# Performance work log

Hardware: AMD Instinct MI355X
Metric: run time of the kernel (lower is better)

Reference implementation:

```python
import jax, jax.numpy as jnp
import numpy as np

N = 50000   # nodes
E = 800000  # edges
D = 128     # input_dim
H = 128     # hidden_dim
C = 40      # output_dim (classes)


def setup_inputs() -> dict:
    key = jax.random.key(0)
    ks = jax.random.split(key, 8)
    x = jax.random.normal(ks[0], (N, D), dtype=jnp.float32)
    edge_index = jax.random.randint(ks[1], (2, E), 0, N, dtype=jnp.int32)
    sD = 1.0 / np.sqrt(D)
    sH = 1.0 / np.sqrt(H)
    W1 = jax.random.uniform(ks[2], (D, H), jnp.float32, -sD, sD)
    b1 = jnp.zeros((H,), jnp.float32)
    W2 = jax.random.uniform(ks[3], (H, H), jnp.float32, -sH, sH)
    b2 = jnp.zeros((H,), jnp.float32)
    W3 = jax.random.uniform(ks[4], (H, C), jnp.float32, -sH, sH)
    b3 = jnp.zeros((C,), jnp.float32)
    return {"x": x, "edge_index": edge_index,
            "W1": W1, "b1": b1, "W2": W2, "b2": b2, "W3": W3, "b3": b3}


def reference(x, edge_index, W1, b1, W2, b2, W3, b3):
    # GCNConv: out = D^{-1/2} (A + I) D^{-1/2} (x @ W) + b
    src = edge_index[0]
    dst = edge_index[1]
    loop = jnp.arange(N, dtype=src.dtype)
    src_f = jnp.concatenate([src, loop])  # [E+N] with self-loops
    dst_f = jnp.concatenate([dst, loop])
    deg = jax.ops.segment_sum(jnp.ones(E + N, x.dtype), dst_f, num_segments=N)
    dinv = jax.lax.rsqrt(jnp.maximum(deg, 1.0))  # deg >= 1 due to self-loops
    norm = dinv[src_f] * dinv[dst_f]  # [E+N]

    def conv(h, W, b):
        h = h @ W                       # [N, F_out]
        msg = h[src_f] * norm[:, None]  # [E+N, F_out] gathered messages
        return jax.ops.segment_sum(msg, dst_f, num_segments=N) + b

    h = jax.nn.relu(conv(x, W1, b1))
    h = jax.nn.relu(conv(h, W2, b2))  # dropout is identity in eval mode
    return conv(h, W3, b3)
```

## Files before the change

kernel.cpp:

```cpp
#include <hip/hip_runtime.h>

typedef unsigned short ushort_t;
typedef unsigned int uint_t;


__global__ void k_deg_count(const int* __restrict__ ei, int* __restrict__ deg, int E) {
    int e = blockIdx.x * blockDim.x + threadIdx.x;
    if (e < E) atomicAdd(&deg[ei[E + e]], 1);
}

__global__ void k_bsum(const int* __restrict__ deg, int* __restrict__ bsum, int n) {
    __shared__ int s[256];
    int t = threadIdx.x;
    int i = blockIdx.x * 256 + t;
    s[t] = (i < n) ? deg[i] : 0;
    __syncthreads();
    for (int off = 128; off > 0; off >>= 1) {
        if (t < off) s[t] += s[t + off];
        __syncthreads();
    }
    if (t == 0) bsum[blockIdx.x] = s[0];
}

__global__ void k_bscan(int* __restrict__ bsum, int* __restrict__ tot, int nb) {
    __shared__ int s[1024];
    int t = threadIdx.x;
    int v = (t < nb) ? bsum[t] : 0;
    s[t] = v;
    __syncthreads();
    for (int off = 1; off < 1024; off <<= 1) {
        int u = (t >= off) ? s[t - off] : 0;
        __syncthreads();
        s[t] += u;
        __syncthreads();
    }
    if (t < nb) bsum[t] = s[t] - v;
    if (t == nb - 1) tot[0] = s[t];
}

__global__ void k_rowptr(const int* __restrict__ deg, const int* __restrict__ bsum,
                         int* __restrict__ rowptr, int* __restrict__ cursor,
                         float* __restrict__ dinv, int n) {
    __shared__ int s[256];
    int t = threadIdx.x;
    int i = blockIdx.x * 256 + t;
    int v = (i < n) ? deg[i] : 0;
    s[t] = v;
    __syncthreads();
    for (int off = 1; off < 256; off <<= 1) {
        int u = (t >= off) ? s[t - off] : 0;
        __syncthreads();
        s[t] += u;
        __syncthreads();
    }
    if (i < n) {
        int ex = bsum[blockIdx.x] + s[t] - v;
        rowptr[i] = ex;
        cursor[i] = ex;
        dinv[i] = rsqrtf((float)(v + 1));
    }
}

__global__ __launch_bounds__(256) void k_fill(const int* __restrict__ ei,
                                              int* __restrict__ cursor,
                                              const float* __restrict__ dinv,
                                              int2* __restrict__ csr, int E, int n) {
    const int xcd = blockIdx.x & 7;
    const int e = (blockIdx.x >> 3) * 256 + threadIdx.x;
    if (e >= E) return;
    int d = ei[E + e];
    const int lo = (int)(((long long)xcd * n) >> 3);
    const int hi = (int)(((long long)(xcd + 1) * n) >> 3);
    if (d < lo || d >= hi) return;
    int s = ei[e];
    int pos = atomicAdd(&cursor[d], 1);
    int2 p;
    p.x = s;
    p.y = __float_as_int(dinv[s] * dinv[d]);
    csr[pos] = p;
}

__device__ __forceinline__ ushort_t f2bf_rne(float f) {
    uint_t u = __float_as_uint(f);
    u += 0x7fffu + ((u >> 16) & 1u);
    return (ushort_t)(u >> 16);
}
__device__ __forceinline__ float bflo(uint_t u) {
    return __uint_as_float(u << 16);
}
__device__ __forceinline__ float bfhi(uint_t u) {
    return __uint_as_float(u & 0xffff0000u);
}

__global__ __launch_bounds__(256) void k_gemm128(const float* __restrict__ X,
                                                 const float* __restrict__ W,
                                                 ushort_t* __restrict__ Y, int N) {
    __shared__ float sX[32][132];
    __shared__ float sW[32][128];
    const int tid = threadIdx.x;
    const int bm = blockIdx.x * 128;
    const int m0 = (tid >> 4) * 8;
    const int c4 = (tid & 15) * 4;
    const int xf = tid & 7;
    float acc[8][8] = {};
    for (int k0 = 0; k0 < 128; k0 += 32) {
        #pragma unroll
        for (int it = 0; it < 4; ++it) {
            int i = tid + it * 256;
            int row = bm + (i >> 3);
            int rc = min(row, N - 1);
            float4 v = *(const float4*)(X + (size_t)rc * 128 + k0 + xf * 4);
            int m = i >> 3;
            sX[xf * 4 + 0][m] = v.x;
            sX[xf * 4 + 1][m] = v.y;
            sX[xf * 4 + 2][m] = v.z;
            sX[xf * 4 + 3][m] = v.w;
        }
        #pragma unroll
        for (int it = 0; it < 4; ++it) {
            int i = tid + it * 256;
            int wr = i >> 5;
            int wf = i & 31;
            *(float4*)(&sW[wr][wf * 4]) =
                *(const float4*)(W + (size_t)(k0 + wr) * 128 + wf * 4);
        }
        __syncthreads();
        #pragma unroll
        for (int kk = 0; kk < 32; ++kk) {
            float4 a0 = *(const float4*)(&sX[kk][m0]);
            float4 a1 = *(const float4*)(&sX[kk][m0 + 4]);
            float4 b0 = *(const float4*)(&sW[kk][c4]);
            float4 b1 = *(const float4*)(&sW[kk][64 + c4]);
            float av[8] = {a0.x, a0.y, a0.z, a0.w, a1.x, a1.y, a1.z, a1.w};
            float bv[8] = {b0.x, b0.y, b0.z, b0.w, b1.x, b1.y, b1.z, b1.w};
            #pragma unroll
            for (int r = 0; r < 8; ++r)
                #pragma unroll
                for (int c = 0; c < 8; ++c)
                    acc[r][c] = fmaf(av[r], bv[c], acc[r][c]);
        }
        __syncthreads();
    }
    #pragma unroll
    for (int r = 0; r < 8; ++r) {
        int row = bm + m0 + r;
        if (row < N) {
            ushort4 o0 = {f2bf_rne(acc[r][0]), f2bf_rne(acc[r][1]),
                          f2bf_rne(acc[r][2]), f2bf_rne(acc[r][3])};
            ushort4 o1 = {f2bf_rne(acc[r][4]), f2bf_rne(acc[r][5]),
                          f2bf_rne(acc[r][6]), f2bf_rne(acc[r][7])};
            *(ushort4*)(Y + (size_t)row * 128 + c4)      = o0;
            *(ushort4*)(Y + (size_t)row * 128 + 64 + c4) = o1;
        }
    }
}

__global__ __launch_bounds__(256) void k_gemm40(const float* __restrict__ X,
                                                const float* __restrict__ W,
                                                ushort_t* __restrict__ Y, int N) {
    __shared__ float sX[32][132];
    __shared__ float sW[32][40];
    const int tid = threadIdx.x;
    const int bm = blockIdx.x * 128;
    const int m0 = (tid >> 3) * 4;
    const int n0 = (tid & 7) * 5;
    const int xf = tid & 7;
    float acc[4][5] = {};
    for (int k0 = 0; k0 < 128; k0 += 32) {
        #pragma unroll
        for (int it = 0; it < 4; ++it) {
            int i = tid + it * 256;
            int row = bm + (i >> 3);
            int rc = min(row, N - 1);
            float4 v = *(const float4*)(X + (size_t)rc * 128 + k0 + xf * 4);
            int m = i >> 3;
            sX[xf * 4 + 0][m] = v.x;
            sX[xf * 4 + 1][m] = v.y;
            sX[xf * 4 + 2][m] = v.z;
            sX[xf * 4 + 3][m] = v.w;
        }
        for (int i = tid; i < 320; i += 256) {
            int wr = i / 10;
            int wf = i - wr * 10;
            *(float4*)(&sW[wr][wf * 4]) =
                *(const float4*)(W + (size_t)(k0 + wr) * 40 + wf * 4);
        }
        __syncthreads();
        #pragma unroll
        for (int kk = 0; kk < 32; ++kk) {
            float4 a = *(const float4*)(&sX[kk][m0]);
            float av[4] = {a.x, a.y, a.z, a.w};
            #pragma unroll
            for (int c = 0; c < 5; ++c) {
                float b = sW[kk][n0 + c];
                #pragma unroll
                for (int r = 0; r < 4; ++r)
                    acc[r][c] = fmaf(av[r], b, acc[r][c]);
            }
        }
        __syncthreads();
    }
    #pragma unroll
    for (int r = 0; r < 4; ++r) {
        int row = bm + m0 + r;
        if (row < N) {
            #pragma unroll
            for (int c = 0; c < 5; ++c)
                Y[(size_t)row * 64 + n0 + c] = f2bf_rne(acc[r][c]);
        }
    }
}

template <bool RELU>
__global__ __launch_bounds__(256) void k_agg128(
        const ushort_t* __restrict__ XW, const int* __restrict__ rowptr,
        const int2* __restrict__ csr, const float* __restrict__ dinv,
        const float* __restrict__ bias, float* __restrict__ out, int n) {
    const int lane = threadIdx.x & 63;
    const int wv = __builtin_amdgcn_readfirstlane(threadIdx.x >> 6);
    const int d = blockIdx.x * 4 + wv;
    if (d >= n) return;
    const uint_t* xw = (const uint_t*)XW;
    float dv = dinv[d];
    float w0 = dv * dv;
    uint_t sq = xw[(size_t)d * 64 + lane];
    float2 a;
    a.x = w0 * bflo(sq);
    a.y = w0 * bfhi(sq);
    int j = rowptr[d], end = rowptr[d + 1];
    for (; j + 8 <= end; j += 8) {
        int2 p0 = csr[j + 0], p1 = csr[j + 1], p2 = csr[j + 2], p3 = csr[j + 3];
        int2 p4 = csr[j + 4], p5 = csr[j + 5], p6 = csr[j + 6], p7 = csr[j + 7];
        uint_t u0 = xw[(size_t)p0.x * 64 + lane];
        uint_t u1 = xw[(size_t)p1.x * 64 + lane];
        uint_t u2 = xw[(size_t)p2.x * 64 + lane];
        uint_t u3 = xw[(size_t)p3.x * 64 + lane];
        uint_t u4 = xw[(size_t)p4.x * 64 + lane];
        uint_t u5 = xw[(size_t)p5.x * 64 + lane];
        uint_t u6 = xw[(size_t)p6.x * 64 + lane];
        uint_t u7 = xw[(size_t)p7.x * 64 + lane];
        float w0e = __int_as_float(p0.y), w1e = __int_as_float(p1.y);
        float w2e = __int_as_float(p2.y), w3e = __int_as_float(p3.y);
        float w4e = __int_as_float(p4.y), w5e = __int_as_float(p5.y);
        float w6e = __int_as_float(p6.y), w7e = __int_as_float(p7.y);
        a.x = fmaf(w0e, bflo(u0), a.x); a.y = fmaf(w0e, bfhi(u0), a.y);
        a.x = fmaf(w1e, bflo(u1), a.x); a.y = fmaf(w1e, bfhi(u1), a.y);
        a.x = fmaf(w2e, bflo(u2), a.x); a.y = fmaf(w2e, bfhi(u2), a.y);
        a.x = fmaf(w3e, bflo(u3), a.x); a.y = fmaf(w3e, bfhi(u3), a.y);
        a.x = fmaf(w4e, bflo(u4), a.x); a.y = fmaf(w4e, bfhi(u4), a.y);
        a.x = fmaf(w5e, bflo(u5), a.x); a.y = fmaf(w5e, bfhi(u5), a.y);
        a.x = fmaf(w6e, bflo(u6), a.x); a.y = fmaf(w6e, bfhi(u6), a.y);
        a.x = fmaf(w7e, bflo(u7), a.x); a.y = fmaf(w7e, bfhi(u7), a.y);
    }
    for (; j < end; ++j) {
        int2 p = csr[j];
        float we = __int_as_float(p.y);
        uint_t u = xw[(size_t)p.x * 64 + lane];
        a.x = fmaf(we, bflo(u), a.x);
        a.y = fmaf(we, bfhi(u), a.y);
    }
    float2 b = ((const float2*)bias)[lane];
    a.x += b.x; a.y += b.y;
    if (RELU) {
        a.x = fmaxf(a.x, 0.f);
        a.y = fmaxf(a.y, 0.f);
    }
    ((float2*)out)[(size_t)d * 64 + lane] = a;
}

__global__ __launch_bounds__(256) void k_agg40(
        const ushort_t* __restrict__ XW, const int* __restrict__ rowptr,
        const int2* __restrict__ csr, const float* __restrict__ dinv,
        const float* __restrict__ bias, float* __restrict__ out, int n) {
    const int lane = threadIdx.x & 31;
    const int sub  = threadIdx.x >> 5;
    const int d = blockIdx.x * 8 + sub;
    if (d >= n || lane >= 20) return;
    const uint_t* xw = (const uint_t*)XW;
    float dv = dinv[d];
    float w0 = dv * dv;
    uint_t sq = xw[(size_t)d * 32 + lane];
    float2 a;
    a.x = w0 * bflo(sq);
    a.y = w0 * bfhi(sq);
    int j = rowptr[d], end = rowptr[d + 1];
    for (; j + 4 <= end; j += 4) {
        int2 p0 = csr[j + 0], p1 = csr[j + 1], p2 = csr[j + 2], p3 = csr[j + 3];
        uint_t u0 = xw[(size_t)p0.x * 32 + lane];
        uint_t u1 = xw[(size_t)p1.x * 32 + lane];
        uint_t u2 = xw[(size_t)p2.x * 32 + lane];
        uint_t u3 = xw[(size_t)p3.x * 32 + lane];
        float w0e = __int_as_float(p0.y), w1e = __int_as_float(p1.y);
        float w2e = __int_as_float(p2.y), w3e = __int_as_float(p3.y);
        a.x = fmaf(w0e, bflo(u0), a.x); a.y = fmaf(w0e, bfhi(u0), a.y);
        a.x = fmaf(w1e, bflo(u1), a.x); a.y = fmaf(w1e, bfhi(u1), a.y);
        a.x = fmaf(w2e, bflo(u2), a.x); a.y = fmaf(w2e, bfhi(u2), a.y);
        a.x = fmaf(w3e, bflo(u3), a.x); a.y = fmaf(w3e, bfhi(u3), a.y);
    }
    for (; j < end; ++j) {
        int2 p = csr[j];
        float we = __int_as_float(p.y);
        uint_t u = xw[(size_t)p.x * 32 + lane];
        a.x = fmaf(we, bflo(u), a.x);
        a.y = fmaf(we, bfhi(u), a.y);
    }
    float2 b = ((const float2*)bias)[lane];
    a.x += b.x; a.y += b.y;
    ((float2*)out)[(size_t)d * 20 + lane] = a;
}

static inline int cdiv(long long a, int b) { return (int)((a + b - 1) / b); }

extern "C" void kernel_launch(void* const* d_in, const int* in_sizes, int n_in,
                              void* d_out, int out_size, void* d_ws, size_t ws_size,
                              hipStream_t stream) {
    const float* x  = (const float*)d_in[0];
    const int*   ei = (const int*)d_in[1];
    const float* W1 = (const float*)d_in[2];
    const float* b1 = (const float*)d_in[3];
    const float* W2 = (const float*)d_in[4];
    const float* b2 = (const float*)d_in[5];
    const float* W3 = (const float*)d_in[6];
    const float* b3 = (const float*)d_in[7];
    float* out = (float*)d_out;

    const int N = in_sizes[0] / 128;
    const int E = in_sizes[1] / 2;

    char* ws = (char*)d_ws;
    int*   deg    = (int*)ws;                 ws += (size_t)N * 4;
    int*   rowptr = (int*)ws;                 ws += (size_t)(N + 1) * 4;
    int*   cursor = (int*)ws;                 ws += (size_t)N * 4;
    float* dinv   = (float*)ws;               ws += (size_t)N * 4;
    int*   bsum   = (int*)ws;                 ws += (size_t)1024 * 4;
    ws = (char*)(((uintptr_t)ws + 127) & ~(uintptr_t)127);
    int2*  csr    = (int2*)ws;                ws += (size_t)E * 8;
    char*  bufA   = ws;                       ws += (size_t)N * 128 * 4;
    float* bufB   = (float*)ws;

    const int BT = 256;
    const int nb = cdiv(N, 256);

    hipMemsetAsync(deg, 0, (size_t)N * 4, stream);
    k_deg_count<<<cdiv(E, BT), BT, 0, stream>>>(ei, deg, E);
    k_bsum<<<nb, 256, 0, stream>>>(deg, bsum, N);
    k_bscan<<<1, 1024, 0, stream>>>(bsum, rowptr + N, nb);
    k_rowptr<<<nb, 256, 0, stream>>>(deg, bsum, rowptr, cursor, dinv, N);
    k_fill<<<cdiv(E, BT) * 8, 256, 0, stream>>>(ei, cursor, dinv, csr, E, N);

    k_gemm128<<<cdiv(N, 128), 256, 0, stream>>>(x, W1, (ushort_t*)bufA, N);
    k_agg128<true><<<cdiv(N, 4), 256, 0, stream>>>((const ushort_t*)bufA, rowptr, csr, dinv, b1, bufB, N);
    k_gemm128<<<cdiv(N, 128), 256, 0, stream>>>(bufB, W2, (ushort_t*)bufA, N);
    k_agg128<true><<<cdiv(N, 4), 256, 0, stream>>>((const ushort_t*)bufA, rowptr, csr, dinv, b2, bufB, N);
    k_gemm40<<<cdiv(N, 128), 256, 0, stream>>>(bufB, W3, (ushort_t*)bufA, N);
    k_agg40<<<cdiv(N, 8), 256, 0, stream>>>((const ushort_t*)bufA, rowptr, csr, dinv, b3, out, N);
}
```

Baseline: 321.8 us.

## Merge three-pass scan into single-pass decoupled lookback; deepen aggregation unroll

```diff
diff --git a/kernel.cpp b/kernel.cpp
--- a/kernel.cpp
+++ b/kernel.cpp
@@ -9,41 +9,14 @@
     if (e < E) atomicAdd(&deg[ei[E + e]], 1);
 }
 
-__global__ void k_bsum(const int* __restrict__ deg, int* __restrict__ bsum, int n) {
+__global__ __launch_bounds__(256) void k_scan(
+        const int* __restrict__ deg, unsigned long long* __restrict__ partials,
+        int* __restrict__ rowptr, int* __restrict__ cursor,
+        float* __restrict__ dinv, int n) {
     __shared__ int s[256];
-    int t = threadIdx.x;
-    int i = blockIdx.x * 256 + t;
-    s[t] = (i < n) ? deg[i] : 0;
-    __syncthreads();
-    for (int off = 128; off > 0; off >>= 1) {
-        if (t < off) s[t] += s[t + off];
-        __syncthreads();
-    }
-    if (t == 0) bsum[blockIdx.x] = s[0];
-}
-
-__global__ void k_bscan(int* __restrict__ bsum, int* __restrict__ tot, int nb) {
-    __shared__ int s[1024];
-    int t = threadIdx.x;
-    int v = (t < nb) ? bsum[t] : 0;
-    s[t] = v;
-    __syncthreads();
-    for (int off = 1; off < 1024; off <<= 1) {
-        int u = (t >= off) ? s[t - off] : 0;
-        __syncthreads();
-        s[t] += u;
-        __syncthreads();
-    }
-    if (t < nb) bsum[t] = s[t] - v;
-    if (t == nb - 1) tot[0] = s[t];
-}
-
-__global__ void k_rowptr(const int* __restrict__ deg, const int* __restrict__ bsum,
-                         int* __restrict__ rowptr, int* __restrict__ cursor,
-                         float* __restrict__ dinv, int n) {
-    __shared__ int s[256];
-    int t = threadIdx.x;
-    int i = blockIdx.x * 256 + t;
+    __shared__ int sprefix;
+    const int b = blockIdx.x, t = threadIdx.x;
+    const int i = b * 256 + t;
     int v = (i < n) ? deg[i] : 0;
     s[t] = v;
     __syncthreads();
@@ -53,11 +26,32 @@
         s[t] += u;
         __syncthreads();
     }
+    if (t == 0) {
+        unsigned long long bs = (unsigned long long)s[255];
+        __hip_atomic_store(&partials[b], (bs << 2) | 1ull,
+                           __ATOMIC_RELEASE, __HIP_MEMORY_SCOPE_AGENT);
+        long long acc = 0;
+        for (int k = b - 1; k >= 0; ) {
+            unsigned long long p = __hip_atomic_load(&partials[k],
+                    __ATOMIC_ACQUIRE, __HIP_MEMORY_SCOPE_AGENT);
+            unsigned st = (unsigned)(p & 3ull);
+            if (st == 0) continue;
+            acc += (long long)(p >> 2);
+            if (st == 2) break;
+            --k;
+        }
+        __hip_atomic_store(&partials[b],
+                (((unsigned long long)(acc + (long long)bs)) << 2) | 2ull,
+                __ATOMIC_RELEASE, __HIP_MEMORY_SCOPE_AGENT);
+        sprefix = (int)acc;
+    }
+    __syncthreads();
     if (i < n) {
-        int ex = bsum[blockIdx.x] + s[t] - v;
+        int ex = sprefix + s[t] - v;
         rowptr[i] = ex;
         cursor[i] = ex;
         dinv[i] = rsqrtf((float)(v + 1));
+        if (i == n - 1) rowptr[n] = ex + v;
     }
 }
 
@@ -228,29 +222,33 @@
     a.x = w0 * bflo(sq);
     a.y = w0 * bfhi(sq);
     int j = rowptr[d], end = rowptr[d + 1];
+    for (; j + 16 <= end; j += 16) {
+        int2 p[16];
+        #pragma unroll
+        for (int q = 0; q < 16; ++q) p[q] = csr[j + q];
+        uint_t u[16];
+        #pragma unroll
+        for (int q = 0; q < 16; ++q) u[q] = xw[(size_t)p[q].x * 64 + lane];
+        #pragma unroll
+        for (int q = 0; q < 16; ++q) {
+            float we = __int_as_float(p[q].y);
+            a.x = fmaf(we, bflo(u[q]), a.x);
+            a.y = fmaf(we, bfhi(u[q]), a.y);
+        }
+    }
     for (; j + 8 <= end; j += 8) {
-        int2 p0 = csr[j + 0], p1 = csr[j + 1], p2 = csr[j + 2], p3 = csr[j + 3];
-        int2 p4 = csr[j + 4], p5 = csr[j + 5], p6 = csr[j + 6], p7 = csr[j + 7];
-        uint_t u0 = xw[(size_t)p0.x * 64 + lane];
-        uint_t u1 = xw[(size_t)p1.x * 64 + lane];
-        uint_t u2 = xw[(size_t)p2.x * 64 + lane];
-        uint_t u3 = xw[(size_t)p3.x * 64 + lane];
-        uint_t u4 = xw[(size_t)p4.x * 64 + lane];
-        uint_t u5 = xw[(size_t)p5.x * 64 + lane];
-        uint_t u6 = xw[(size_t)p6.x * 64 + lane];
-        uint_t u7 = xw[(size_t)p7.x * 64 + lane];
-        float w0e = __int_as_float(p0.y), w1e = __int_as_float(p1.y);
-        float w2e = __int_as_float(p2.y), w3e = __int_as_float(p3.y);
-        float w4e = __int_as_float(p4.y), w5e = __int_as_float(p5.y);
-        float w6e = __int_as_float(p6.y), w7e = __int_as_float(p7.y);
-        a.x = fmaf(w0e, bflo(u0), a.x); a.y = fmaf(w0e, bfhi(u0), a.y);
-        a.x = fmaf(w1e, bflo(u1), a.x); a.y = fmaf(w1e, bfhi(u1), a.y);
-        a.x = fmaf(w2e, bflo(u2), a.x); a.y = fmaf(w2e, bfhi(u2), a.y);
-        a.x = fmaf(w3e, bflo(u3), a.x); a.y = fmaf(w3e, bfhi(u3), a.y);
-        a.x = fmaf(w4e, bflo(u4), a.x); a.y = fmaf(w4e, bfhi(u4), a.y);
-        a.x = fmaf(w5e, bflo(u5), a.x); a.y = fmaf(w5e, bfhi(u5), a.y);
-        a.x = fmaf(w6e, bflo(u6), a.x); a.y = fmaf(w6e, bfhi(u6), a.y);
-        a.x = fmaf(w7e, bflo(u7), a.x); a.y = fmaf(w7e, bfhi(u7), a.y);
+        int2 p[8];
+        #pragma unroll
+        for (int q = 0; q < 8; ++q) p[q] = csr[j + q];
+        uint_t u[8];
+        #pragma unroll
+        for (int q = 0; q < 8; ++q) u[q] = xw[(size_t)p[q].x * 64 + lane];
+        #pragma unroll
+        for (int q = 0; q < 8; ++q) {
+            float we = __int_as_float(p[q].y);
+            a.x = fmaf(we, bflo(u[q]), a.x);
+            a.y = fmaf(we, bfhi(u[q]), a.y);
+        }
     }
     for (; j < end; ++j) {
         int2 p = csr[j];
@@ -272,9 +270,9 @@
         const ushort_t* __restrict__ XW, const int* __restrict__ rowptr,
         const int2* __restrict__ csr, const float* __restrict__ dinv,
         const float* __restrict__ bias, float* __restrict__ out, int n) {
-    const int lane = threadIdx.x & 31;
-    const int sub  = threadIdx.x >> 5;
-    const int d = blockIdx.x * 8 + sub;
+    const int lane = threadIdx.x & 63;
+    const int wv = __builtin_amdgcn_readfirstlane(threadIdx.x >> 6);
+    const int d = blockIdx.x * 4 + wv;
     if (d >= n || lane >= 20) return;
     const uint_t* xw = (const uint_t*)XW;
     float dv = dinv[d];
@@ -284,18 +282,33 @@
     a.x = w0 * bflo(sq);
     a.y = w0 * bfhi(sq);
     int j = rowptr[d], end = rowptr[d + 1];
-    for (; j + 4 <= end; j += 4) {
-        int2 p0 = csr[j + 0], p1 = csr[j + 1], p2 = csr[j + 2], p3 = csr[j + 3];
-        uint_t u0 = xw[(size_t)p0.x * 32 + lane];
-        uint_t u1 = xw[(size_t)p1.x * 32 + lane];
-        uint_t u2 = xw[(size_t)p2.x * 32 + lane];
-        uint_t u3 = xw[(size_t)p3.x * 32 + lane];
-        float w0e = __int_as_float(p0.y), w1e = __int_as_float(p1.y);
-        float w2e = __int_as_float(p2.y), w3e = __int_as_float(p3.y);
-        a.x = fmaf(w0e, bflo(u0), a.x); a.y = fmaf(w0e, bfhi(u0), a.y);
-        a.x = fmaf(w1e, bflo(u1), a.x); a.y = fmaf(w1e, bfhi(u1), a.y);
-        a.x = fmaf(w2e, bflo(u2), a.x); a.y = fmaf(w2e, bfhi(u2), a.y);
-        a.x = fmaf(w3e, bflo(u3), a.x); a.y = fmaf(w3e, bfhi(u3), a.y);
+    for (; j + 16 <= end; j += 16) {
+        int2 p[16];
+        #pragma unroll
+        for (int q = 0; q < 16; ++q) p[q] = csr[j + q];
+        uint_t u[16];
+        #pragma unroll
+        for (int q = 0; q < 16; ++q) u[q] = xw[(size_t)p[q].x * 32 + lane];
+        #pragma unroll
+        for (int q = 0; q < 16; ++q) {
+            float we = __int_as_float(p[q].y);
+            a.x = fmaf(we, bflo(u[q]), a.x);
+            a.y = fmaf(we, bfhi(u[q]), a.y);
+        }
+    }
+    for (; j + 8 <= end; j += 8) {
+        int2 p[8];
+        #pragma unroll
+        for (int q = 0; q < 8; ++q) p[q] = csr[j + q];
+        uint_t u[8];
+        #pragma unroll
+        for (int q = 0; q < 8; ++q) u[q] = xw[(size_t)p[q].x * 32 + lane];
+        #pragma unroll
+        for (int q = 0; q < 8; ++q) {
+            float we = __int_as_float(p[q].y);
+            a.x = fmaf(we, bflo(u[q]), a.x);
+            a.y = fmaf(we, bfhi(u[q]), a.y);
+        }
     }
     for (; j < end; ++j) {
         int2 p = csr[j];
@@ -326,26 +339,25 @@
 
     const int N = in_sizes[0] / 128;
     const int E = in_sizes[1] / 2;
+    const int nb = cdiv(N, 256);
 
     char* ws = (char*)d_ws;
     int*   deg    = (int*)ws;                 ws += (size_t)N * 4;
+    unsigned long long* partials = (unsigned long long*)ws;
+                                              ws += (size_t)nb * 8;
     int*   rowptr = (int*)ws;                 ws += (size_t)(N + 1) * 4;
     int*   cursor = (int*)ws;                 ws += (size_t)N * 4;
     float* dinv   = (float*)ws;               ws += (size_t)N * 4;
-    int*   bsum   = (int*)ws;                 ws += (size_t)1024 * 4;
     ws = (char*)(((uintptr_t)ws + 127) & ~(uintptr_t)127);
     int2*  csr    = (int2*)ws;                ws += (size_t)E * 8;
     char*  bufA   = ws;                       ws += (size_t)N * 128 * 4;
     float* bufB   = (float*)ws;
 
     const int BT = 256;
-    const int nb = cdiv(N, 256);
-
-    hipMemsetAsync(deg, 0, (size_t)N * 4, stream);
+
+    hipMemsetAsync(deg, 0, (size_t)N * 4 + (size_t)nb * 8, stream);
     k_deg_count<<<cdiv(E, BT), BT, 0, stream>>>(ei, deg, E);
-    k_bsum<<<nb, 256, 0, stream>>>(deg, bsum, N);
-    k_bscan<<<1, 1024, 0, stream>>>(bsum, rowptr + N, nb);
-    k_rowptr<<<nb, 256, 0, stream>>>(deg, bsum, rowptr, cursor, dinv, N);
+    k_scan<<<nb, 256, 0, stream>>>(deg, partials, rowptr, cursor, dinv, N);
     k_fill<<<cdiv(E, BT) * 8, 256, 0, stream>>>(ei, cursor, dinv, csr, E, N);
 
     k_gemm128<<<cdiv(N, 128), 256, 0, stream>>>(x, W1, (ushort_t*)bufA, N);
@@ -353,5 +365,5 @@
     k_gemm128<<<cdiv(N, 128), 256, 0, stream>>>(bufB, W2, (ushort_t*)bufA, N);
     k_agg128<true><<<cdiv(N, 4), 256, 0, stream>>>((const ushort_t*)bufA, rowptr, csr, dinv, b2, bufB, N);
     k_gemm40<<<cdiv(N, 128), 256, 0, stream>>>(bufB, W3, (ushort_t*)bufA, N);
-    k_agg40<<<cdiv(N, 8), 256, 0, stream>>>((const ushort_t*)bufA, rowptr, csr, dinv, b3, out, N);
-}
+    k_agg40<<<cdiv(N, 4), 256, 0, stream>>>((const ushort_t*)bufA, rowptr, csr, dinv, b3, out, N);
+}
```

Result: slower. 358.3 us (+11.4%).

## Replace three-kernel prefix scan with single-pass decoupled look-back scan

Applied to the files above, without the earlier changes.

```diff
diff --git a/kernel.cpp b/kernel.cpp
--- a/kernel.cpp
+++ b/kernel.cpp
@@ -9,41 +9,14 @@
     if (e < E) atomicAdd(&deg[ei[E + e]], 1);
 }
 
-__global__ void k_bsum(const int* __restrict__ deg, int* __restrict__ bsum, int n) {
+__global__ __launch_bounds__(256) void k_scan(
+        const int* __restrict__ deg, unsigned long long* __restrict__ partials,
+        int* __restrict__ rowptr, int* __restrict__ cursor,
+        float* __restrict__ dinv, int n) {
     __shared__ int s[256];
-    int t = threadIdx.x;
-    int i = blockIdx.x * 256 + t;
-    s[t] = (i < n) ? deg[i] : 0;
-    __syncthreads();
-    for (int off = 128; off > 0; off >>= 1) {
-        if (t < off) s[t] += s[t + off];
-        __syncthreads();
-    }
-    if (t == 0) bsum[blockIdx.x] = s[0];
-}
-
-__global__ void k_bscan(int* __restrict__ bsum, int* __restrict__ tot, int nb) {
-    __shared__ int s[1024];
-    int t = threadIdx.x;
-    int v = (t < nb) ? bsum[t] : 0;
-    s[t] = v;
-    __syncthreads();
-    for (int off = 1; off < 1024; off <<= 1) {
-        int u = (t >= off) ? s[t - off] : 0;
-        __syncthreads();
-        s[t] += u;
-        __syncthreads();
-    }
-    if (t < nb) bsum[t] = s[t] - v;
-    if (t == nb - 1) tot[0] = s[t];
-}
-
-__global__ void k_rowptr(const int* __restrict__ deg, const int* __restrict__ bsum,
-                         int* __restrict__ rowptr, int* __restrict__ cursor,
-                         float* __restrict__ dinv, int n) {
-    __shared__ int s[256];
-    int t = threadIdx.x;
-    int i = blockIdx.x * 256 + t;
+    __shared__ int sprefix;
+    const int b = blockIdx.x, t = threadIdx.x;
+    const int i = b * 256 + t;
     int v = (i < n) ? deg[i] : 0;
     s[t] = v;
     __syncthreads();
@@ -53,11 +26,57 @@
         s[t] += u;
         __syncthreads();
     }
+    if (t == 0) {
+        __hip_atomic_store(&partials[b],
+                ((unsigned long long)s[255] << 2) | 1ull,
+                __ATOMIC_RELEASE, __HIP_MEMORY_SCOPE_AGENT);
+        if (b == 0) {
+            __hip_atomic_store(&partials[0],
+                    ((unsigned long long)s[255] << 2) | 2ull,
+                    __ATOMIC_RELEASE, __HIP_MEMORY_SCOPE_AGENT);
+            sprefix = 0;
+        }
+    }
+    if (b > 0 && t < 64) {
+        int acc = 0;
+        int k = b - 1;
+        for (;;) {
+            int idx = k - t;
+            unsigned long long p;
+            unsigned st;
+            do {
+                if (idx >= 0) {
+                    p = __hip_atomic_load(&partials[idx],
+                            __ATOMIC_ACQUIRE, __HIP_MEMORY_SCOPE_AGENT);
+                } else {
+                    p = 2ull;
+                }
+                st = (unsigned)(p & 3ull);
+            } while (st == 0);
+            unsigned long long bal = __ballot(st == 2);
+            int L = (bal != 0) ? (__ffsll((unsigned long long)bal) - 1) : 64;
+            int val = (int)(p >> 2);
+            int contrib = (t <= L) ? val : 0;
+            #pragma unroll
+            for (int o = 32; o > 0; o >>= 1) contrib += __shfl_down(contrib, o);
+            if (t == 0) acc += contrib;
+            if (L < 64) break;
+            k -= 64;
+        }
+        if (t == 0) {
+            __hip_atomic_store(&partials[b],
+                    (((unsigned long long)(acc + s[255])) << 2) | 2ull,
+                    __ATOMIC_RELEASE, __HIP_MEMORY_SCOPE_AGENT);
+            sprefix = acc;
+        }
+    }
+    __syncthreads();
     if (i < n) {
-        int ex = bsum[blockIdx.x] + s[t] - v;
+        int ex = sprefix + s[t] - v;
         rowptr[i] = ex;
         cursor[i] = ex;
         dinv[i] = rsqrtf((float)(v + 1));
+        if (i == n - 1) rowptr[n] = ex + v;
     }
 }
 
@@ -326,26 +345,25 @@
 
     const int N = in_sizes[0] / 128;
     const int E = in_sizes[1] / 2;
+    const int nb = cdiv(N, 256);
 
     char* ws = (char*)d_ws;
     int*   deg    = (int*)ws;                 ws += (size_t)N * 4;
+    unsigned long long* partials = (unsigned long long*)ws;
+                                              ws += (size_t)nb * 8;
     int*   rowptr = (int*)ws;                 ws += (size_t)(N + 1) * 4;
     int*   cursor = (int*)ws;                 ws += (size_t)N * 4;
     float* dinv   = (float*)ws;               ws += (size_t)N * 4;
-    int*   bsum   = (int*)ws;                 ws += (size_t)1024 * 4;
     ws = (char*)(((uintptr_t)ws + 127) & ~(uintptr_t)127);
     int2*  csr    = (int2*)ws;                ws += (size_t)E * 8;
     char*  bufA   = ws;                       ws += (size_t)N * 128 * 4;
     float* bufB   = (float*)ws;
 
     const int BT = 256;
-    const int nb = cdiv(N, 256);
-
-    hipMemsetAsync(deg, 0, (size_t)N * 4, stream);
+
+    hipMemsetAsync(deg, 0, (size_t)N * 4 + (size_t)nb * 8, stream);
     k_deg_count<<<cdiv(E, BT), BT, 0, stream>>>(ei, deg, E);
-    k_bsum<<<nb, 256, 0, stream>>>(deg, bsum, N);
-    k_bscan<<<1, 1024, 0, stream>>>(bsum, rowptr + N, nb);
-    k_rowptr<<<nb, 256, 0, stream>>>(deg, bsum, rowptr, cursor, dinv, N);
+    k_scan<<<nb, 256, 0, stream>>>(deg, partials, rowptr, cursor, dinv, N);
     k_fill<<<cdiv(E, BT) * 8, 256, 0, stream>>>(ei, cursor, dinv, csr, E, N);
 
     k_gemm128<<<cdiv(N, 128), 256, 0, stream>>>(x, W1, (ushort_t*)bufA, N);
```

Measured after the change: 328.1 us. About the same (+2.0%).
